# Kernel optimization log

Hardware: AMD Instinct MI355X
Metric: run time of the kernel (lower is better)

Reference implementation:

```python
import jax, jax.numpy as jnp
import numpy as np

D = 131072  # inner feature dim
N = 84      # 4*(1 + 4*(1 + 4)) entries emitted by calc_probs


def calc_probs(logits):
    # softmax over the 4 logits, then emit, in original nested-loop order:
    # for i: p_i, then for j: p_i*p_j followed by p_i*p_j*p_k for k in 0..3
    p = jax.nn.softmax(logits)                      # (4,)
    pairs = p[:, None] * p[None, :]                 # (4,4)
    triples = pairs[:, :, None] * p[None, None, :]  # (4,4,4)
    inner = jnp.concatenate([pairs[:, :, None], triples], axis=2)  # (4,4,5)
    full = jnp.concatenate([p[:, None], inner.reshape(4, 20)], axis=1)  # (4,21)
    return full.reshape(N)  # (84,)


def setup_inputs() -> dict:
    key = jax.random.key(0)
    ks = jax.random.split(key, 6)
    return {
        "BEV": jax.random.normal(ks[0], (1,), dtype=jnp.float32),
        "ST0": jax.random.normal(ks[1], (N, D), dtype=jnp.float32),
        "Weight0": jax.random.normal(ks[2], (N, D, 1), dtype=jnp.float32),
        "ST1": jax.random.normal(ks[3], (N, D), dtype=jnp.float32),
        "Weight1": jax.random.normal(ks[4], (N, D, 1), dtype=jnp.float32),
        "Problem": 1,
        "probs0": jnp.array([2.0327, 1.0198, 1.024, 0.9935], dtype=jnp.float32),
        "probs1": jnp.array([2.6661, 1.0168, 1.02, 0.9971], dtype=jnp.float32),
        "probs2": jnp.array([2.8173, 1.016, 1.0189, 0.9978], dtype=jnp.float32),
        "probs3": jnp.array([2.9183, 1.0154, 1.0181, 0.9981], dtype=jnp.float32),
        "probs4": jnp.array([2.9689, 1.0151, 1.0177, 0.9983], dtype=jnp.float32),
        "pBEV": jnp.array([0.1822], dtype=jnp.float32),
        "pB": jnp.array([3.1475], dtype=jnp.float32),
    }


def reference(BEV, ST0, Weight0, ST1, Weight1, Problem,
              probs0, probs1, probs2, probs3, probs4, pBEV, pB):
    p0 = calc_probs(probs0)
    p1 = calc_probs(probs1)
    p2 = calc_probs(probs2)
    p3 = calc_probs(probs3)
    p4 = calc_probs(probs4)
    # fused sigmoid + per-row dot, replacing the Python loop over 84 rows
    bev = pBEV * BEV  # (1,)
    tmp0 = jnp.einsum('id,id->i', jax.nn.sigmoid(pB * (bev + ST0)), Weight0[..., 0])  # (84,)
    tmp1 = jnp.einsum('id,id->i', jax.nn.sigmoid(pB * (bev + ST1)), Weight1[..., 0])  # (84,)
    vals = jnp.stack([p0 @ tmp0, p1 @ tmp1, p2 @ tmp1, p3 @ tmp1, p4 @ tmp1])
    return jnp.mean(vals)
```

## Files before the change

kernel.cpp:

```cpp
#include <hip/hip_runtime.h>
#include <hip/hip_bf16.h>


#define D_DIM      131072
#define N_ROWS     84
#define ROW_F4     (D_DIM / 4)
#define TENSOR_F4  (N_ROWS * ROW_F4)
#define BLOCKS     1792
#define T0_BLOCKS  896
#define F4_PER_BLOCK 3072
#define F4_PER_THREAD 12

__device__ inline float prob_entry(const float* __restrict__ logits, int t) {
    float l0 = logits[0], l1 = logits[1], l2 = logits[2], l3 = logits[3];
    float m  = fmaxf(fmaxf(l0, l1), fmaxf(l2, l3));
    float e0 = __expf(l0 - m), e1 = __expf(l1 - m);
    float e2 = __expf(l2 - m), e3 = __expf(l3 - m);
    float inv = 1.0f / (e0 + e1 + e2 + e3);
    float p[4] = {e0 * inv, e1 * inv, e2 * inv, e3 * inv};
    int i = t / 21;
    int r = t - i * 21;
    if (r == 0) return p[i];
    r -= 1;
    int j = r / 5;
    int s = r - j * 5;
    float v = p[i] * p[j];
    return (s == 0) ? v : v * p[s - 1];
}

__global__ __launch_bounds__(256, 4) void probsnet_main(
    const float* __restrict__ BEV,
    const float* __restrict__ ST0, const float* __restrict__ W0,
    const float* __restrict__ ST1, const float* __restrict__ W1,
    const float* __restrict__ probs0, const float* __restrict__ probs1,
    const float* __restrict__ probs2, const float* __restrict__ probs3,
    const float* __restrict__ probs4,
    const float* __restrict__ pBEV, const float* __restrict__ pB,
    float* __restrict__ partials)
{
    const int bid    = blockIdx.x;
    const int t      = threadIdx.x;
    const int tensor = (bid >= T0_BLOCKS) ? 1 : 0;
    const int fb     = bid * F4_PER_BLOCK - tensor * TENSOR_F4;

    const float bev = pBEV[0] * BEV[0];
    const float pb  = pB[0];

    __shared__ float wrow[N_ROWS];
    if (t < N_ROWS) {
        wrow[t] = (tensor == 0)
            ? prob_entry(probs0, t)
            : prob_entry(probs1, t) + prob_entry(probs2, t)
            + prob_entry(probs3, t) + prob_entry(probs4, t);
    }
    __syncthreads();

    const float4* __restrict__ stp =
        (const float4*)(tensor ? ST1 : ST0) + fb + t;
    const float4* __restrict__ wpp =
        (const float4*)(tensor ? W1 : W0) + fb + t;

    float4 sb[4], wb[4];
    #pragma unroll
    for (int k = 0; k < 4; ++k) {
        sb[k] = stp[k * 256];
        wb[k] = wpp[k * 256];
    }

    float acc = 0.0f;
    #pragma unroll
    for (int k = 0; k < F4_PER_THREAD; ++k) {
        float4 s4 = sb[k & 3];
        float4 w4 = wb[k & 3];
        if (k + 4 < F4_PER_THREAD) {
            sb[k & 3] = stp[(k + 4) * 256];
            wb[k & 3] = wpp[(k + 4) * 256];
        }
        float sum;
        sum  = w4.x / (1.0f + __expf(-pb * (bev + s4.x)));
        sum += w4.y / (1.0f + __expf(-pb * (bev + s4.y)));
        sum += w4.z / (1.0f + __expf(-pb * (bev + s4.z)));
        sum += w4.w / (1.0f + __expf(-pb * (bev + s4.w)));
        const int row = (fb + t + k * 256) >> 15;
        acc = fmaf(wrow[row], sum, acc);
    }

    #pragma unroll
    for (int off = 32; off > 0; off >>= 1)
        acc += __shfl_down(acc, off, 64);

    __shared__ float red[4];
    const int wave = t >> 6;
    const int lane = t & 63;
    if (lane == 0) red[wave] = acc;
    __syncthreads();

    if (t == 0)
        partials[bid] = red[0] + red[1] + red[2] + red[3];
}

__global__ __launch_bounds__(256) void probsnet_reduce(
    const float* __restrict__ partials, float* __restrict__ out)
{
    const int t = threadIdx.x;
    float acc = 0.0f;
    #pragma unroll
    for (int k = 0; k < BLOCKS / 256; ++k)
        acc += partials[t + k * 256];

    #pragma unroll
    for (int off = 32; off > 0; off >>= 1)
        acc += __shfl_down(acc, off, 64);

    __shared__ float red[4];
    const int wave = t >> 6;
    const int lane = t & 63;
    if (lane == 0) red[wave] = acc;
    __syncthreads();

    if (t == 0)
        out[0] = (red[0] + red[1] + red[2] + red[3]) * 0.2f;
}

extern "C" void kernel_launch(void* const* d_in, const int* in_sizes, int n_in,
                              void* d_out, int out_size, void* d_ws, size_t ws_size,
                              hipStream_t stream) {
    const float* BEV    = (const float*)d_in[0];
    const float* ST0    = (const float*)d_in[1];
    const float* W0     = (const float*)d_in[2];
    const float* ST1    = (const float*)d_in[3];
    const float* W1     = (const float*)d_in[4];
    const float* probs0 = (const float*)d_in[6];
    const float* probs1 = (const float*)d_in[7];
    const float* probs2 = (const float*)d_in[8];
    const float* probs3 = (const float*)d_in[9];
    const float* probs4 = (const float*)d_in[10];
    const float* pBEV   = (const float*)d_in[11];
    const float* pB     = (const float*)d_in[12];

    float* partials = (float*)d_ws;
    float* out      = (float*)d_out;

    probsnet_main<<<BLOCKS, 256, 0, stream>>>(
        BEV, ST0, W0, ST1, W1,
        probs0, probs1, probs2, probs3, probs4,
        pBEV, pB, partials);

    probsnet_reduce<<<1, 256, 0, stream>>>(partials, out);
}
```

Baseline: 202.4 us.

## Shrink per-block work, hoist all loads, defer row weights to block epilogue

Measured after the change: 202.0 us. About the same (-0.2%).

```diff
diff --git a/kernel.cpp b/kernel.cpp
--- a/kernel.cpp
+++ b/kernel.cpp
@@ -2,14 +2,14 @@
 #include <hip/hip_bf16.h>
 
 
-#define D_DIM      131072
-#define N_ROWS     84
-#define ROW_F4     (D_DIM / 4)
-#define TENSOR_F4  (N_ROWS * ROW_F4)
-#define BLOCKS     1792
-#define T0_BLOCKS  896
-#define F4_PER_BLOCK 3072
-#define F4_PER_THREAD 12
+#define D_DIM         131072
+#define N_ROWS        84
+#define ROW_F4        (D_DIM / 4)
+#define TENSOR_F4     (N_ROWS * ROW_F4)
+#define F4_PER_BLOCK  768
+#define T0_BLOCKS     (TENSOR_F4 / F4_PER_BLOCK)
+#define BLOCKS        (2 * T0_BLOCKS)
+#define F4_PER_THREAD 3
 
 __device__ inline float prob_entry(const float* __restrict__ logits, int t) {
     float l0 = logits[0], l1 = logits[1], l2 = logits[2], l3 = logits[3];
@@ -28,6 +28,11 @@
     return (s == 0) ? v : v * p[s - 1];
 }
 
+__device__ inline float sigdot(float w, float s, float a, float ab) {
+    float e = __builtin_amdgcn_exp2f(fmaf(a, s, ab));
+    return w * __builtin_amdgcn_rcpf(1.0f + e);
+}
+
 __global__ __launch_bounds__(256, 4) void probsnet_main(
     const float* __restrict__ BEV,
     const float* __restrict__ ST0, const float* __restrict__ W0,
@@ -41,62 +46,71 @@
     const int bid    = blockIdx.x;
     const int t      = threadIdx.x;
     const int tensor = (bid >= T0_BLOCKS) ? 1 : 0;
-    const int fb     = bid * F4_PER_BLOCK - tensor * TENSOR_F4;
+    const int fb     = (bid - tensor * T0_BLOCKS) * F4_PER_BLOCK;
 
+    const float pb  = pB[0];
     const float bev = pBEV[0] * BEV[0];
-    const float pb  = pB[0];
-
-    __shared__ float wrow[N_ROWS];
-    if (t < N_ROWS) {
-        wrow[t] = (tensor == 0)
-            ? prob_entry(probs0, t)
-            : prob_entry(probs1, t) + prob_entry(probs2, t)
-            + prob_entry(probs3, t) + prob_entry(probs4, t);
-    }
-    __syncthreads();
+    const float a   = -pb * 1.4426950408889634f;
+    const float ab  = a * bev;
 
     const float4* __restrict__ stp =
         (const float4*)(tensor ? ST1 : ST0) + fb + t;
     const float4* __restrict__ wpp =
         (const float4*)(tensor ? W1 : W0) + fb + t;
 
-    float4 sb[4], wb[4];
-    #pragma unroll
-    for (int k = 0; k < 4; ++k) {
-        sb[k] = stp[k * 256];
-        wb[k] = wpp[k * 256];
-    }
-
-    float acc = 0.0f;
+    float4 sv[F4_PER_THREAD], wv[F4_PER_THREAD];
     #pragma unroll
     for (int k = 0; k < F4_PER_THREAD; ++k) {
-        float4 s4 = sb[k & 3];
-        float4 w4 = wb[k & 3];
-        if (k + 4 < F4_PER_THREAD) {
-            sb[k & 3] = stp[(k + 4) * 256];
-            wb[k & 3] = wpp[(k + 4) * 256];
-        }
-        float sum;
-        sum  = w4.x / (1.0f + __expf(-pb * (bev + s4.x)));
-        sum += w4.y / (1.0f + __expf(-pb * (bev + s4.y)));
-        sum += w4.z / (1.0f + __expf(-pb * (bev + s4.z)));
-        sum += w4.w / (1.0f + __expf(-pb * (bev + s4.w)));
-        const int row = (fb + t + k * 256) >> 15;
-        acc = fmaf(wrow[row], sum, acc);
+        sv[k] = stp[k * 256];
+        wv[k] = wpp[k * 256];
+    }
+    __builtin_amdgcn_sched_barrier(0);
+
+    const int row_lo = fb >> 15;
+    const int row_hi = (fb + F4_PER_BLOCK - 1) >> 15;
+    const int rb     = (row_hi > row_lo) ? (row_hi << 15) : 0x7FFFFFFF;
+
+    float acc_lo = 0.0f, acc_hi = 0.0f;
+    #pragma unroll
+    for (int k = 0; k < F4_PER_THREAD; ++k) {
+        float c;
+        c  = sigdot(wv[k].x, sv[k].x, a, ab);
+        c += sigdot(wv[k].y, sv[k].y, a, ab);
+        c += sigdot(wv[k].z, sv[k].z, a, ab);
+        c += sigdot(wv[k].w, sv[k].w, a, ab);
+        const bool hi = (fb + t + k * 256) >= rb;
+        acc_lo += hi ? 0.0f : c;
+        acc_hi += hi ? c : 0.0f;
     }
 
     #pragma unroll
-    for (int off = 32; off > 0; off >>= 1)
-        acc += __shfl_down(acc, off, 64);
+    for (int off = 32; off > 0; off >>= 1) {
+        acc_lo += __shfl_down(acc_lo, off, 64);
+        acc_hi += __shfl_down(acc_hi, off, 64);
+    }
 
-    __shared__ float red[4];
+    __shared__ float red_lo[4], red_hi[4];
     const int wave = t >> 6;
     const int lane = t & 63;
-    if (lane == 0) red[wave] = acc;
+    if (lane == 0) { red_lo[wave] = acc_lo; red_hi[wave] = acc_hi; }
     __syncthreads();
 
-    if (t == 0)
-        partials[bid] = red[0] + red[1] + red[2] + red[3];
+    if (t == 0) {
+        const float S_lo = red_lo[0] + red_lo[1] + red_lo[2] + red_lo[3];
+        const float S_hi = red_hi[0] + red_hi[1] + red_hi[2] + red_hi[3];
+        float w_lo, w_hi = 0.0f;
+        if (tensor == 0) {
+            w_lo = prob_entry(probs0, row_lo);
+            if (row_hi > row_lo) w_hi = prob_entry(probs0, row_hi);
+        } else {
+            w_lo = prob_entry(probs1, row_lo) + prob_entry(probs2, row_lo)
+                 + prob_entry(probs3, row_lo) + prob_entry(probs4, row_lo);
+            if (row_hi > row_lo)
+                w_hi = prob_entry(probs1, row_hi) + prob_entry(probs2, row_hi)
+                     + prob_entry(probs3, row_hi) + prob_entry(probs4, row_hi);
+        }
+        partials[bid] = w_lo * S_lo + w_hi * S_hi;
+    }
 }
 
 __global__ __launch_bounds__(256) void probsnet_reduce(
```

## Use grid-stride loop over both tensors with exp2/rcp sigmoid intrinsics

Applied to the files above, without the earlier changes.

New measurement: 204.2 us. Within noise of the previous version (+0.9%).

```diff
diff --git a/kernel.cpp b/kernel.cpp
--- a/kernel.cpp
+++ b/kernel.cpp
@@ -6,10 +6,11 @@
 #define N_ROWS     84
 #define ROW_F4     (D_DIM / 4)
 #define TENSOR_F4  (N_ROWS * ROW_F4)
-#define BLOCKS     1792
-#define T0_BLOCKS  896
-#define F4_PER_BLOCK 3072
-#define F4_PER_THREAD 12
+#define TOTAL_F4   (2 * TENSOR_F4)
+#define GRID       2048
+#define NTHREADS   (GRID * 256)
+
+typedef float f32x4 __attribute__((ext_vector_type(4)));
 
 __device__ inline float prob_entry(const float* __restrict__ logits, int t) {
     float l0 = logits[0], l1 = logits[1], l2 = logits[2], l3 = logits[3];
@@ -28,7 +29,12 @@
     return (s == 0) ? v : v * p[s - 1];
 }
 
-__global__ __launch_bounds__(256, 4) void probsnet_main(
+__device__ inline float sigdot(float w, float s, float a, float ab) {
+    float e = __builtin_amdgcn_exp2f(fmaf(a, s, ab));
+    return w * __builtin_amdgcn_rcpf(1.0f + e);
+}
+
+__global__ __launch_bounds__(256, 8) void probsnet_main(
     const float* __restrict__ BEV,
     const float* __restrict__ ST0, const float* __restrict__ W0,
     const float* __restrict__ ST1, const float* __restrict__ W1,
@@ -38,51 +44,42 @@
     const float* __restrict__ pBEV, const float* __restrict__ pB,
     float* __restrict__ partials)
 {
-    const int bid    = blockIdx.x;
-    const int t      = threadIdx.x;
-    const int tensor = (bid >= T0_BLOCKS) ? 1 : 0;
-    const int fb     = bid * F4_PER_BLOCK - tensor * TENSOR_F4;
+    const int t    = threadIdx.x;
+    const int gtid = blockIdx.x * 256 + t;
 
+    const float pb  = pB[0];
     const float bev = pBEV[0] * BEV[0];
-    const float pb  = pB[0];
+    const float a   = -pb * 1.4426950408889634f;
+    const float ab  = a * bev;
 
-    __shared__ float wrow[N_ROWS];
+    __shared__ float wrow[2 * N_ROWS];
     if (t < N_ROWS) {
-        wrow[t] = (tensor == 0)
-            ? prob_entry(probs0, t)
-            : prob_entry(probs1, t) + prob_entry(probs2, t)
-            + prob_entry(probs3, t) + prob_entry(probs4, t);
+        wrow[t] = prob_entry(probs0, t);
+    } else if (t < 2 * N_ROWS) {
+        const int r = t - N_ROWS;
+        wrow[t] = prob_entry(probs1, r) + prob_entry(probs2, r)
+                + prob_entry(probs3, r) + prob_entry(probs4, r);
     }
     __syncthreads();
 
-    const float4* __restrict__ stp =
-        (const float4*)(tensor ? ST1 : ST0) + fb + t;
-    const float4* __restrict__ wpp =
-        (const float4*)(tensor ? W1 : W0) + fb + t;
-
-    float4 sb[4], wb[4];
-    #pragma unroll
-    for (int k = 0; k < 4; ++k) {
-        sb[k] = stp[k * 256];
-        wb[k] = wpp[k * 256];
-    }
+    const f32x4* __restrict__ st0 = (const f32x4*)ST0;
+    const f32x4* __restrict__ w0  = (const f32x4*)W0;
+    const f32x4* __restrict__ st1 = (const f32x4*)ST1;
+    const f32x4* __restrict__ w1  = (const f32x4*)W1;
 
     float acc = 0.0f;
-    #pragma unroll
-    for (int k = 0; k < F4_PER_THREAD; ++k) {
-        float4 s4 = sb[k & 3];
-        float4 w4 = wb[k & 3];
-        if (k + 4 < F4_PER_THREAD) {
-            sb[k & 3] = stp[(k + 4) * 256];
-            wb[k & 3] = wpp[(k + 4) * 256];
-        }
-        float sum;
-        sum  = w4.x / (1.0f + __expf(-pb * (bev + s4.x)));
-        sum += w4.y / (1.0f + __expf(-pb * (bev + s4.y)));
-        sum += w4.z / (1.0f + __expf(-pb * (bev + s4.z)));
-        sum += w4.w / (1.0f + __expf(-pb * (bev + s4.w)));
-        const int row = (fb + t + k * 256) >> 15;
-        acc = fmaf(wrow[row], sum, acc);
+    for (int idx = gtid; idx < TOTAL_F4; idx += NTHREADS) {
+        const int  tensor = (idx >= TENSOR_F4) ? 1 : 0;
+        const int  il     = idx - tensor * TENSOR_F4;
+        const f32x4 s4 = tensor ? st1[il] : st0[il];
+        const f32x4 w4 = tensor ? w1[il]  : w0[il];
+        const float w  = wrow[(il >> 15) + tensor * N_ROWS];
+        float c4;
+        c4  = sigdot(w4[0], s4[0], a, ab);
+        c4 += sigdot(w4[1], s4[1], a, ab);
+        c4 += sigdot(w4[2], s4[2], a, ab);
+        c4 += sigdot(w4[3], s4[3], a, ab);
+        acc = fmaf(w, c4, acc);
     }
 
     #pragma unroll
@@ -96,7 +93,7 @@
     __syncthreads();
 
     if (t == 0)
-        partials[bid] = red[0] + red[1] + red[2] + red[3];
+        partials[blockIdx.x] = red[0] + red[1] + red[2] + red[3];
 }
 
 __global__ __launch_bounds__(256) void probsnet_reduce(
@@ -105,7 +102,7 @@
     const int t = threadIdx.x;
     float acc = 0.0f;
     #pragma unroll
-    for (int k = 0; k < BLOCKS / 256; ++k)
+    for (int k = 0; k < GRID / 256; ++k)
         acc += partials[t + k * 256];
 
     #pragma unroll
@@ -141,7 +138,7 @@
     float* partials = (float*)d_ws;
     float* out      = (float*)d_out;
 
-    probsnet_main<<<BLOCKS, 256, 0, stream>>>(
+    probsnet_main<<<GRID, 256, 0, stream>>>(
         BEV, ST0, W0, ST1, W1,
         probs0, probs1, probs2, probs3, probs4,
         pBEV, pB, partials);
```
